# Performance work log

Hardware: AMD Instinct MI355X
Metric: run time of the kernel (lower is better)

Reference implementation:

```python
import jax, jax.numpy as jnp
import numpy as np

B, S, D, H = 1, 2048, 1024, 16
HD = D // H
THRESHOLD_PCT = 0.95
SPARSITY = 0.9
TOPK = max(1, int(S * (1.0 - SPARSITY)))  # 204


def setup_inputs() -> dict:
    key = jax.random.key(0)
    ks = jax.random.split(key, 6)
    inp = {
        'x': jax.random.normal(ks[0], (B, S, D), dtype=jnp.float32),
        'Wq': jax.random.normal(ks[1], (D, D), dtype=jnp.float32) * 0.02,
        'bq': jnp.zeros((D,), jnp.float32),
        'Wk': jax.random.normal(ks[2], (D, D), dtype=jnp.float32) * 0.02,
        'bk': jnp.zeros((D,), jnp.float32),
        'Wv': jax.random.normal(ks[3], (D, D), dtype=jnp.float32) * 0.02,
        'bv': jnp.zeros((D,), jnp.float32),
        'Wo': jax.random.normal(ks[4], (D, D), dtype=jnp.float32) * 0.02,
        'bo': jnp.zeros((D,), jnp.float32),
    }
    return inp


def _heads(t):  # [B,S,D] -> [B,H,S,HD]
    return t.reshape(B, S, H, HD).transpose(0, 2, 1, 3)


def reference(x, Wq, bq, Wk, bk, Wv, bv, Wo, bo):
    q = _heads(x @ Wq + bq)
    k = _heads(x @ Wk + bk)
    v = _heads(x @ Wv + bv)
    scores = jnp.einsum('bhqd,bhkd->bhqk', q, k) / jnp.sqrt(jnp.float32(HD))

    # --- dynamic threshold mask (per batch,head quantile over all S*S scores) ---
    flat = scores.reshape(B, H, S * S)
    thr = jnp.quantile(flat, THRESHOLD_PCT, axis=-1)[..., None, None]  # [B,H,1,1]
    thresh_mask = scores >= thr
    # fallback: if kept fraction exceeds (1 - sparsity_ratio), use per-row top-k
    cond = jnp.mean(thresh_mask.astype(scores.dtype)) > (1.0 - SPARSITY)
    kth = jax.lax.top_k(scores, TOPK)[0][..., -1:]  # k-th largest per row
    topk_mask = scores >= kth
    mask = jnp.where(cond, topk_mask, thresh_mask)

    masked = jnp.where(mask, scores, -jnp.inf)
    attn = jax.nn.softmax(masked, axis=-1)
    out = jnp.einsum('bhqk,bhkd->bhqd', attn, v)
    out = out.transpose(0, 2, 1, 3).reshape(B, S, D)
    return out @ Wo + bo
```

## Files before the change

### kernel.cpp

```cpp
#include <hip/hip_runtime.h>
#include <math.h>

#define SS 2048
#define DD 1024
#define HH 16
#define CAPC 49152u
#define LCAP 2048

#define K_A 3984587u
#define K_B 3984588u
#define QFRAC 0.85f
#define WSCALE 2048.0f
#define WSCALE_INV (1.0f/2048.0f)
#define ESHIFT 4.0f
#define PLANE 2097152

typedef _Float16 f16x8 __attribute__((ext_vector_type(8)));
typedef _Float16 f16x4 __attribute__((ext_vector_type(4)));
typedef float    f32x4 __attribute__((ext_vector_type(4)));

__device__ __forceinline__ unsigned sortkey(float f) {
  unsigned b = __float_as_uint(f);
  return (b & 0x80000000u) ? ~b : (b | 0x80000000u);
}
__device__ __forceinline__ float inv_sortkey(unsigned u) {
  unsigned b = (u & 0x80000000u) ? (u ^ 0x80000000u) : ~u;
  return __uint_as_float(b);
}

__global__ __launch_bounds__(256) void split_x(const float* __restrict__ x,
                                               _Float16* __restrict__ xh,
                                               _Float16* __restrict__ xl)
{
  const int i = blockIdx.x * 256 + threadIdx.x;
  float4 v = ((const float4*)x)[i];
  float vv[4] = {v.x, v.y, v.z, v.w};
  f16x4 h, l;
#pragma unroll
  for (int j = 0; j < 4; ++j) {
    _Float16 hh = (_Float16)vv[j];
    h[j] = hh;
    l[j] = (_Float16)(vv[j] - (float)hh);
  }
  ((f16x4*)xh)[i] = h;
  ((f16x4*)xl)[i] = l;
}

__global__ __launch_bounds__(256) void split_wT(const float* __restrict__ Wq,
                                                const float* __restrict__ Wk,
                                                const float* __restrict__ Wv,
                                                const float* __restrict__ Wo,
                                                _Float16* __restrict__ wplanes)
{
  const int z = blockIdx.z;
  const float* W = (z == 0) ? Wq : (z == 1) ? Wk : (z == 2) ? Wv : Wo;
  _Float16* WhT = wplanes + (size_t)(2*z)     * (1024*1024);
  _Float16* WlT = wplanes + (size_t)(2*z + 1) * (1024*1024);
  __shared__ float tile[64][65];
  const int t  = threadIdx.x;
  const int r  = t >> 2;
  const int c0 = (t & 3) * 16;
  const int k0 = blockIdx.y * 64;
  const int n0 = blockIdx.x * 64;
#pragma unroll
  for (int j = 0; j < 4; ++j) {
    float4 v = *(const float4*)&W[(size_t)(k0 + r) * 1024 + n0 + c0 + j*4];
    tile[r][c0+j*4+0] = v.x; tile[r][c0+j*4+1] = v.y;
    tile[r][c0+j*4+2] = v.z; tile[r][c0+j*4+3] = v.w;
  }
  __syncthreads();
  f16x8 h0, h1, l0, l1;
#pragma unroll
  for (int j = 0; j < 8; ++j) {
    float v = tile[c0 + j][r] * WSCALE;
    _Float16 h = (_Float16)v;
    h0[j] = h; l0[j] = (_Float16)(v - (float)h);
  }
#pragma unroll
  for (int j = 0; j < 8; ++j) {
    float v = tile[c0 + 8 + j][r] * WSCALE;
    _Float16 h = (_Float16)v;
    h1[j] = h; l1[j] = (_Float16)(v - (float)h);
  }
  const size_t o = (size_t)(n0 + r) * 1024 + k0 + c0;
  *(f16x8*)&WhT[o]     = h0;
  *(f16x8*)&WhT[o + 8] = h1;
  *(f16x8*)&WlT[o]     = l0;
  *(f16x8*)&WlT[o + 8] = l1;
}

__device__ __forceinline__ void gemm_mfma_part(const _Float16* __restrict__ Ah,
                                               const _Float16* __restrict__ Al,
                                               const _Float16* __restrict__ BhT,
                                               const _Float16* __restrict__ BlT,
                                               float* __restrict__ pout,
                                               int bm, int bn, int kh)
{
  const int wave = threadIdx.x >> 6, lane = threadIdx.x & 63;
  const int wr = wave >> 1, wc = wave & 1;
  const int m0 = bm * 128 + wr * 64;
  const int n0 = bn * 128 + wc * 64;
  const int lr = lane & 15;
  const int ko = lane >> 4;

  f32x4 acc[4][4];
#pragma unroll
  for (int i = 0; i < 4; ++i)
#pragma unroll
    for (int j = 0; j < 4; ++j) acc[i][j] = (f32x4){0.f, 0.f, 0.f, 0.f};

  for (int kk = kh*16; kk < kh*16 + 16; ++kk) {
    const int kof = kk*32 + ko*8;
    f16x8 aH[4], aL[4], bH[4], bL[4];
#pragma unroll
    for (int i = 0; i < 4; ++i) {
      const size_t aoff = (size_t)(m0 + i*16 + lr) * 1024 + kof;
      aH[i] = *(const f16x8*)(Ah + aoff);
      aL[i] = *(const f16x8*)(Al + aoff);
      const size_t boff = (size_t)(n0 + i*16 + lr) * 1024 + kof;
      bH[i] = *(const f16x8*)(BhT + boff);
      bL[i] = *(const f16x8*)(BlT + boff);
    }
#pragma unroll
    for (int i = 0; i < 4; ++i)
#pragma unroll
      for (int j = 0; j < 4; ++j) {
        acc[i][j] = __builtin_amdgcn_mfma_f32_16x16x32_f16(aL[i], bL[j], acc[i][j], 0, 0, 0);
        acc[i][j] = __builtin_amdgcn_mfma_f32_16x16x32_f16(aH[i], bL[j], acc[i][j], 0, 0, 0);
        acc[i][j] = __builtin_amdgcn_mfma_f32_16x16x32_f16(aL[i], bH[j], acc[i][j], 0, 0, 0);
        acc[i][j] = __builtin_amdgcn_mfma_f32_16x16x32_f16(aH[i], bH[j], acc[i][j], 0, 0, 0);
      }
  }

#pragma unroll
  for (int i = 0; i < 4; ++i)
#pragma unroll
    for (int j = 0; j < 4; ++j)
#pragma unroll
      for (int r = 0; r < 4; ++r) {
        const int row = m0 + i*16 + ko*4 + r;
        const int col = n0 + j*16 + lr;
        pout[(size_t)row * 1024 + col] = acc[i][j][r];
      }
}

__global__ __launch_bounds__(256) void gemm_qkv_part(const _Float16* __restrict__ xh,
                                                     const _Float16* __restrict__ xl,
                                                     const _Float16* __restrict__ wplanes,
                                                     float* __restrict__ pbuf)
{
  const int z = blockIdx.z;
  const int g = z >> 1, kh = z & 1;
  const _Float16* BhT = wplanes + (size_t)(2*g)     * (1024*1024);
  const _Float16* BlT = wplanes + (size_t)(2*g + 1) * (1024*1024);
  gemm_mfma_part(xh, xl, BhT, BlT, pbuf + (size_t)z * PLANE,
                 blockIdx.y, blockIdx.x, kh);
}

__global__ __launch_bounds__(256) void gemm_o_part(const _Float16* __restrict__ ctxh,
                                                   const _Float16* __restrict__ ctxl,
                                                   const _Float16* __restrict__ wplanes,
                                                   float* __restrict__ pO)
{
  const int kh = blockIdx.z;
  gemm_mfma_part(ctxh, ctxl,
                 wplanes + (size_t)6 * (1024*1024),
                 wplanes + (size_t)7 * (1024*1024),
                 pO + (size_t)kh * PLANE, blockIdx.y, blockIdx.x, kh);
}

__global__ __launch_bounds__(256) void combine_qk(const float* __restrict__ pbuf,
                                                  const float* __restrict__ bq,
                                                  const float* __restrict__ bk,
                                                  _Float16* __restrict__ Qh,
                                                  _Float16* __restrict__ Ql,
                                                  _Float16* __restrict__ Kh,
                                                  _Float16* __restrict__ Kl)
{
  const int which = blockIdx.y;
  const float* p0 = pbuf + (size_t)(which*2)     * PLANE;
  const float* p1 = pbuf + (size_t)(which*2 + 1) * PLANE;
  const float* bias = which ? bk : bq;
  _Float16* Oh = which ? Kh : Qh;
  _Float16* Ol = which ? Kl : Ql;
  const int i = blockIdx.x * 256 + threadIdx.x;
  const int coloff = (i & 255) * 4;
  float4 a = ((const float4*)p0)[i];
  float4 b = ((const float4*)p1)[i];
  float av[4] = {a.x, a.y, a.z, a.w};
  float bv[4] = {b.x, b.y, b.z, b.w};
  f16x4 h, l;
#pragma unroll
  for (int j = 0; j < 4; ++j) {
    const float val = (av[j] + bv[j]) * WSCALE_INV + bias[coloff + j];
    _Float16 hh = (_Float16)val;
    h[j] = hh;
    l[j] = (_Float16)(val - (float)hh);
  }
  ((f16x4*)Oh)[i] = h;
  ((f16x4*)Ol)[i] = l;
}

__global__ __launch_bounds__(256) void combine_vT(const float* __restrict__ pbuf,
                                                  const float* __restrict__ bv,
                                                  _Float16* __restrict__ VtH,
                                                  _Float16* __restrict__ VtL)
{
  const float* p0 = pbuf + (size_t)4 * PLANE;
  const float* p1 = pbuf + (size_t)5 * PLANE;
  __shared__ float tile[64][65];
  const int t  = threadIdx.x;
  const int d0 = blockIdx.x * 64;
  const int m0 = blockIdx.y * 64;
  {
    const int r  = t >> 2;
    const int c0 = (t & 3) * 16;
#pragma unroll
    for (int j = 0; j < 4; ++j) {
      const size_t o = (size_t)(m0 + r) * 1024 + d0 + c0 + j*4;
      float4 a = *(const float4*)(p0 + o);
      float4 b = *(const float4*)(p1 + o);
      tile[r][c0+j*4+0] = (a.x + b.x) * WSCALE_INV + bv[d0 + c0 + j*4 + 0];
      tile[r][c0+j*4+1] = (a.y + b.y) * WSCALE_INV + bv[d0 + c0 + j*4 + 1];
      tile[r][c0+j*4+2] = (a.z + b.z) * WSCALE_INV + bv[d0 + c0 + j*4 + 2];
      tile[r][c0+j*4+3] = (a.w + b.w) * WSCALE_INV + bv[d0 + c0 + j*4 + 3];
    }
  }
  __syncthreads();
  {
    const int d  = t >> 2;
    const int rg = (t & 3) * 16;
#pragma unroll
    for (int j = 0; j < 4; ++j) {
      f16x4 hv, lv;
#pragma unroll
      for (int r = 0; r < 4; ++r) {
        const float val = tile[rg + j*4 + r][d];
        _Float16 h = (_Float16)val;
        hv[r] = h; lv[r] = (_Float16)(val - (float)h);
      }
      const size_t o = (size_t)(d0 + d) * 2048 + m0 + rg + j*4;
      *(f16x4*)&VtH[o] = hv;
      *(f16x4*)&VtL[o] = lv;
    }
  }
}

__global__ __launch_bounds__(256) void combine_o(const float* __restrict__ pO,
                                                 const float* __restrict__ bo,
                                                 float* __restrict__ out)
{
  const float* p0 = pO;
  const float* p1 = pO + (size_t)1 * PLANE;
  const int i = blockIdx.x * 256 + threadIdx.x;
  const int coloff = (i & 255) * 4;
  float4 a = ((const float4*)p0)[i];
  float4 b = ((const float4*)p1)[i];
  float4 o;
  o.x = (a.x + b.x) * WSCALE_INV + bo[coloff + 0];
  o.y = (a.y + b.y) * WSCALE_INV + bo[coloff + 1];
  o.z = (a.z + b.z) * WSCALE_INV + bo[coloff + 2];
  o.w = (a.w + b.w) * WSCALE_INV + bo[coloff + 3];
  ((float4*)out)[i] = o;
}

__global__ __launch_bounds__(256) void combine_ctx(const float* __restrict__ pctx,
                                                   const float* __restrict__ prs,
                                                   _Float16* __restrict__ ctxh,
                                                   _Float16* __restrict__ ctxl)
{
  const float* p0 = pctx;
  const float* p1 = pctx + (size_t)1 * PLANE;
  const int i = blockIdx.x * 256 + threadIdx.x;
  const int row = i >> 8;
  const int cd  = (i & 255) * 4;
  const int h   = cd >> 6;
  const float rs = prs[h*2048 + row] + prs[32768 + h*2048 + row];
  float4 a = ((const float4*)p0)[i];
  float4 b = ((const float4*)p1)[i];
  float av[4] = {a.x, a.y, a.z, a.w};
  float bv[4] = {b.x, b.y, b.z, b.w};
  f16x4 hh, ll;
#pragma unroll
  for (int j = 0; j < 4; ++j) {
    const float val = (av[j] + bv[j]) / rs;
    _Float16 hv = (_Float16)val;
    hh[j] = hv;
    ll[j] = (_Float16)(val - (float)hv);
  }
  ((f16x4*)ctxh)[i] = hh;
  ((f16x4*)ctxl)[i] = ll;
}

__global__ __launch_bounds__(512) void scores_hist(const _Float16* __restrict__ Qh,
                                                   const _Float16* __restrict__ Ql,
                                                   const _Float16* __restrict__ Kh,
                                                   const _Float16* __restrict__ Kl,
                                                   unsigned* __restrict__ ghist)
{
  const int bn = blockIdx.x, bm = blockIdx.y, h = blockIdx.z;
  const int wave = threadIdx.x >> 6, lane = threadIdx.x & 63;
  const int wr = wave >> 1, wc = wave & 1;
  const int m0 = bm * 256 + wr * 64;
  const int n0 = bn * 128 + wc * 64;
  const int lr = lane & 15;
  const int ko = lane >> 4;

  __shared__ unsigned lh[16384];
  for (int i = threadIdx.x; i < 16384; i += 512) lh[i] = 0;
  __syncthreads();

  f32x4 acc[4][4];
#pragma unroll
  for (int i = 0; i < 4; ++i)
#pragma unroll
    for (int j = 0; j < 4; ++j) acc[i][j] = (f32x4){0.f, 0.f, 0.f, 0.f};

#pragma unroll
  for (int kk = 0; kk < 2; ++kk) {
    f16x8 aH[4], aL[4], bH[4], bL[4];
#pragma unroll
    for (int i = 0; i < 4; ++i) {
      const size_t aoff = (size_t)(m0 + i*16 + lr) * 1024 + h*64 + kk*32 + ko*8;
      aH[i] = *(const f16x8*)(Qh + aoff);
      aL[i] = *(const f16x8*)(Ql + aoff);
      const size_t boff = (size_t)(n0 + i*16 + lr) * 1024 + h*64 + kk*32 + ko*8;
      bH[i] = *(const f16x8*)(Kh + boff);
      bL[i] = *(const f16x8*)(Kl + boff);
    }
#pragma unroll
    for (int i = 0; i < 4; ++i)
#pragma unroll
      for (int j = 0; j < 4; ++j) {
        acc[i][j] = __builtin_amdgcn_mfma_f32_16x16x32_f16(aL[i], bL[j], acc[i][j], 0, 0, 0);
        acc[i][j] = __builtin_amdgcn_mfma_f32_16x16x32_f16(aH[i], bL[j], acc[i][j], 0, 0, 0);
        acc[i][j] = __builtin_amdgcn_mfma_f32_16x16x32_f16(aL[i], bH[j], acc[i][j], 0, 0, 0);
        acc[i][j] = __builtin_amdgcn_mfma_f32_16x16x32_f16(aH[i], bH[j], acc[i][j], 0, 0, 0);
      }
  }

#pragma unroll
  for (int i = 0; i < 4; ++i)
#pragma unroll
    for (int j = 0; j < 4; ++j)
#pragma unroll
      for (int r = 0; r < 4; ++r) {
        const float val = acc[i][j][r] * 0.125f;
        atomicAdd(&lh[sortkey(val) >> 18], 1u);
      }
  __syncthreads();
  unsigned* __restrict__ gh = ghist + (size_t)h * 16384;
  for (int i = threadIdx.x; i < 16384; i += 512) {
    const unsigned c = lh[i];
    if (c) atomicAdd(&gh[i], c);
  }
}

__global__ __launch_bounds__(256) void init14(unsigned* __restrict__ ghist,
                                              unsigned* __restrict__ ccnt)
{
  int i = blockIdx.x * 256 + threadIdx.x;
  for (; i < HH * 16384; i += gridDim.x * 256) ghist[i] = 0;
  if (blockIdx.x == 0 && threadIdx.x < HH) ccnt[threadIdx.x] = 0;
}

__global__ __launch_bounds__(256) void scan14(const unsigned* __restrict__ ghist,
                                              unsigned* __restrict__ state)
{
  const int hh = blockIdx.x;
  const int t = threadIdx.x;
  __shared__ unsigned part[256];
  __shared__ unsigned out[4];
  const unsigned* __restrict__ hb = ghist + (size_t)hh * 16384;
  unsigned s = 0;
  for (int j = 0; j < 64; ++j) s += hb[t*64 + j];
  part[t] = s;
  __syncthreads();
  if (t == 0) {
    unsigned run = 0;
    for (int i = 0; i < 256; ++i) { unsigned tmp = part[i]; part[i] = run; run += tmp; }
  }
  __syncthreads();
  const unsigned cum0 = part[t];
  if (K_A >= cum0 && K_A < cum0 + s) {
    unsigned c2 = cum0;
    for (int j = 0; j < 64; ++j) {
      const unsigned c = hb[t*64 + j];
      if (K_A < c2 + c) {
        const unsigned binA = t*64 + j;
        const unsigned residA = K_A - c2;
        unsigned binB, residB;
        if (residA + 1 < c) { binB = binA; residB = residA + 1; }
        else {
          unsigned bb = binA + 1;
          while (bb < 16384 && hb[bb] == 0) ++bb;
          if (bb >= 16384) bb = 16383;
          binB = bb; residB = 0;
        }
        out[0] = binA; out[1] = residA; out[2] = binB; out[3] = residB;
        break;
      }
      c2 += c;
    }
  }
  __syncthreads();
  if (t < 4) state[hh*4 + t] = out[t];
}

__global__ __launch_bounds__(512) void compact_recompute(const _Float16* __restrict__ Qh,
                                                         const _Float16* __restrict__ Ql,
                                                         const _Float16* __restrict__ Kh,
                                                         const _Float16* __restrict__ Kl,
                                                         const unsigned* __restrict__ state,
                                                         unsigned* __restrict__ cand,
                                                         unsigned* __restrict__ ccnt)
{
  const int bn = blockIdx.x, bm = blockIdx.y, h = blockIdx.z;
  const int wave = threadIdx.x >> 6, lane = threadIdx.x & 63;
  const int wr = wave >> 1, wc = wave & 1;
  const int m0 = bm * 256 + wr * 64;
  const int n0 = bn * 128 + wc * 64;
  const int lr = lane & 15;
  const int ko = lane >> 4;

  __shared__ unsigned lbuf[LCAP];
  __shared__ unsigned lcnt, gbase;
  if (threadIdx.x == 0) lcnt = 0;
  __syncthreads();
  const unsigned binA = state[h*4+0];
  const unsigned binB = state[h*4+2];
  unsigned* __restrict__ mycand = cand + (size_t)h * CAPC;

  f32x4 acc[4][4];
#pragma unroll
  for (int i = 0; i < 4; ++i)
#pragma unroll
    for (int j = 0; j < 4; ++j) acc[i][j] = (f32x4){0.f, 0.f, 0.f, 0.f};

#pragma unroll
  for (int kk = 0; kk < 2; ++kk) {
    f16x8 aH[4], aL[4], bH[4], bL[4];
#pragma unroll
    for (int i = 0; i < 4; ++i) {
      const size_t aoff = (size_t)(m0 + i*16 + lr) * 1024 + h*64 + kk*32 + ko*8;
      aH[i] = *(const f16x8*)(Qh + aoff);
      aL[i] = *(const f16x8*)(Ql + aoff);
      const size_t boff = (size_t)(n0 + i*16 + lr) * 1024 + h*64 + kk*32 + ko*8;
      bH[i] = *(const f16x8*)(Kh + boff);
      bL[i] = *(const f16x8*)(Kl + boff);
    }
#pragma unroll
    for (int i = 0; i < 4; ++i)
#pragma unroll
      for (int j = 0; j < 4; ++j) {
        acc[i][j] = __builtin_amdgcn_mfma_f32_16x16x32_f16(aL[i], bL[j], acc[i][j], 0, 0, 0);
        acc[i][j] = __builtin_amdgcn_mfma_f32_16x16x32_f16(aH[i], bL[j], acc[i][j], 0, 0, 0);
        acc[i][j] = __builtin_amdgcn_mfma_f32_16x16x32_f16(aL[i], bH[j], acc[i][j], 0, 0, 0);
        acc[i][j] = __builtin_amdgcn_mfma_f32_16x16x32_f16(aH[i], bH[j], acc[i][j], 0, 0, 0);
      }
  }

#pragma unroll
  for (int i = 0; i < 4; ++i)
#pragma unroll
    for (int j = 0; j < 4; ++j)
#pragma unroll
      for (int r = 0; r < 4; ++r) {
        const float val = acc[i][j][r] * 0.125f;
        const unsigned u = sortkey(val);
        const unsigned bin = u >> 18;
        if (bin == binA || bin == binB) {
          unsigned id = atomicAdd(&lcnt, 1u);
          if (id < LCAP) lbuf[id] = u;
          else { unsigned g = atomicAdd(&ccnt[h], 1u); if (g < CAPC) mycand[g] = u; }
        }
      }
  __syncthreads();
  const unsigned n = (lcnt < LCAP) ? lcnt : LCAP;
  if (threadIdx.x == 0) gbase = n ? atomicAdd(&ccnt[h], n) : 0u;
  __syncthreads();
  const unsigned gb = gbase;
  for (unsigned i = threadIdx.x; i < n; i += 512)
    if (gb + i < CAPC) mycand[gb + i] = lbuf[i];
}

__global__ __launch_bounds__(256) void final_select_list(const unsigned* __restrict__ cand,
                                                         const unsigned* __restrict__ ccnt,
                                                         const unsigned* __restrict__ state,
                                                         float* __restrict__ thr)
{
  const int hh = blockIdx.x;
  const int t = threadIdx.x;
  __shared__ unsigned hist[256];
  __shared__ unsigned digitS, kresS;
  __shared__ float valS[2];
  unsigned n = ccnt[hh]; if (n > CAPC) n = CAPC;
  const unsigned* __restrict__ list = cand + (size_t)hh * CAPC;
  for (int tgt = 0; tgt < 2; ++tgt) {
    unsigned pfx = state[hh*4 + tgt*2];
    unsigned k   = state[hh*4 + tgt*2 + 1];
    for (int r = 0; r < 3; ++r) {
      const int s = (r == 0) ? 10 : (r == 1) ? 2 : 0;
      const int w = (r == 2) ? 2 : 8;
      const unsigned nb = 1u << w;
      hist[t] = 0;
      __syncthreads();
      for (unsigned i = t; i < n; i += 256) {
        const unsigned u = list[i];
        if ((u >> (s + w)) == pfx) atomicAdd(&hist[(u >> s) & (nb - 1)], 1u);
      }
      __syncthreads();
      if (t == 0) {
        unsigned cum = 0, b = 0;
        for (; b < nb; ++b) { const unsigned c = hist[b]; if (cum + c > k) break; cum += c; }
        if (b == nb) b = nb - 1;
        digitS = b; kresS = k - cum;
      }
      __syncthreads();
      pfx = (pfx << w) | digitS;
      k = kresS;
    }
    if (t == 0) valS[tgt] = inv_sortkey(pfx);
    __syncthreads();
  }
  if (t == 0) thr[hh] = valS[0] + QFRAC * (valS[1] - valS[0]);
}

__global__ __launch_bounds__(256) void flash_pv_sk(const _Float16* __restrict__ Qh,
                                                   const _Float16* __restrict__ Ql,
                                                   const _Float16* __restrict__ Kh,
                                                   const _Float16* __restrict__ Kl,
                                                   const _Float16* __restrict__ VtH,
                                                   const _Float16* __restrict__ VtL,
                                                   const float* __restrict__ thrArr,
                                                   float* __restrict__ pctx,
                                                   float* __restrict__ prs)
{
  const int bm = blockIdx.x;
  const int h  = blockIdx.y;
  const int half = blockIdx.z;
  const int wave = threadIdx.x >> 6, lane = threadIdx.x & 63;
  const int lr = lane & 15;
  const int ko = lane >> 4;
  const int m0 = bm * 64;
  const float thr = thrArr[h];

  __shared__ _Float16 Plds[64][136];
  __shared__ float rsLDS[64][4];

  f16x8 qH[4][2], qL[4][2];
#pragma unroll
  for (int i = 0; i < 4; ++i)
#pragma unroll
    for (int kk = 0; kk < 2; ++kk) {
      const size_t aoff = (size_t)(m0 + i*16 + lr) * 1024 + h*64 + kk*32 + ko*8;
      qH[i][kk] = *(const f16x8*)(Qh + aoff);
      qL[i][kk] = *(const f16x8*)(Ql + aoff);
    }

  f32x4 oacc[4];
#pragma unroll
  for (int i = 0; i < 4; ++i) oacc[i] = (f32x4){0.f, 0.f, 0.f, 0.f};
  float rs[4][4];
#pragma unroll
  for (int i = 0; i < 4; ++i)
#pragma unroll
    for (int r = 0; r < 4; ++r) rs[i][r] = 0.f;

  const int d0 = wave * 16;

  for (int kt = half*8; kt < half*8 + 8; ++kt) {
    const int n0 = kt*128 + wave*32;
    f32x4 sacc[4][2];
#pragma unroll
    for (int i = 0; i < 4; ++i)
#pragma unroll
      for (int j = 0; j < 2; ++j) sacc[i][j] = (f32x4){0.f, 0.f, 0.f, 0.f};

#pragma unroll
    for (int kk = 0; kk < 2; ++kk) {
      f16x8 bH[2], bL[2];
#pragma unroll
      for (int j = 0; j < 2; ++j) {
        const size_t boff = (size_t)(n0 + j*16 + lr) * 1024 + h*64 + kk*32 + ko*8;
        bH[j] = *(const f16x8*)(Kh + boff);
        bL[j] = *(const f16x8*)(Kl + boff);
      }
#pragma unroll
      for (int i = 0; i < 4; ++i)
#pragma unroll
        for (int j = 0; j < 2; ++j) {
          sacc[i][j] = __builtin_amdgcn_mfma_f32_16x16x32_f16(qL[i][kk], bL[j], sacc[i][j], 0, 0, 0);
          sacc[i][j] = __builtin_amdgcn_mfma_f32_16x16x32_f16(qH[i][kk], bL[j], sacc[i][j], 0, 0, 0);
          sacc[i][j] = __builtin_amdgcn_mfma_f32_16x16x32_f16(qL[i][kk], bH[j], sacc[i][j], 0, 0, 0);
          sacc[i][j] = __builtin_amdgcn_mfma_f32_16x16x32_f16(qH[i][kk], bH[j], sacc[i][j], 0, 0, 0);
        }
    }

#pragma unroll
    for (int i = 0; i < 4; ++i)
#pragma unroll
      for (int j = 0; j < 2; ++j)
#pragma unroll
        for (int r = 0; r < 4; ++r) {
          const float val = sacc[i][j][r] * 0.125f;
          const float p = (val >= thr) ? __expf(val - thr - ESHIFT) : 0.f;
          rs[i][r] += p;
          Plds[i*16 + ko*4 + r][wave*32 + j*16 + lr] = (_Float16)p;
        }
    __syncthreads();

#pragma unroll
    for (int kk2 = 0; kk2 < 4; ++kk2) {
      f16x8 pa[4];
#pragma unroll
      for (int i = 0; i < 4; ++i)
        pa[i] = *(const f16x8*)&Plds[i*16 + lr][kk2*32 + ko*8];
      const size_t vo = (size_t)(h*64 + d0 + lr) * 2048 + kt*128 + kk2*32 + ko*8;
      const f16x8 vH = *(const f16x8*)(VtH + vo);
      const f16x8 vL = *(const f16x8*)(VtL + vo);
#pragma unroll
      for (int i = 0; i < 4; ++i) {
        oacc[i] = __builtin_amdgcn_mfma_f32_16x16x32_f16(pa[i], vL, oacc[i], 0, 0, 0);
        oacc[i] = __builtin_amdgcn_mfma_f32_16x16x32_f16(pa[i], vH, oacc[i], 0, 0, 0);
      }
    }
    __syncthreads();
  }

#pragma unroll
  for (int i = 0; i < 4; ++i)
#pragma unroll
    for (int r = 0; r < 4; ++r) {
      float v = rs[i][r];
      v += __shfl_xor(v, 1); v += __shfl_xor(v, 2);
      v += __shfl_xor(v, 4); v += __shfl_xor(v, 8);
      rs[i][r] = v;
    }
  if (lr == 0) {
#pragma unroll
    for (int i = 0; i < 4; ++i)
#pragma unroll
      for (int r = 0; r < 4; ++r)
        rsLDS[i*16 + ko*4 + r][wave] = rs[i][r];
  }
  __syncthreads();

  if (wave == 0 && lr == 0) {
#pragma unroll
    for (int i = 0; i < 4; ++i)
#pragma unroll
      for (int r = 0; r < 4; ++r) {
        const int lrow = i*16 + ko*4 + r;
        prs[half*32768 + h*2048 + m0 + lrow] =
            rsLDS[lrow][0] + rsLDS[lrow][1] + rsLDS[lrow][2] + rsLDS[lrow][3];
      }
  }

  float* __restrict__ pc = pctx + (size_t)half * PLANE;
#pragma unroll
  for (int i = 0; i < 4; ++i)
#pragma unroll
    for (int r = 0; r < 4; ++r) {
      const int lrow = i*16 + ko*4 + r;
      pc[(size_t)(m0 + lrow) * 1024 + h*64 + d0 + lr] = oacc[i][r];
    }
}

extern "C" void kernel_launch(void* const* d_in, const int* in_sizes, int n_in,
                              void* d_out, int out_size, void* d_ws, size_t ws_size,
                              hipStream_t stream)
{
  const float* x  = (const float*)d_in[0];
  const float* Wq = (const float*)d_in[1];
  const float* bq = (const float*)d_in[2];
  const float* Wk = (const float*)d_in[3];
  const float* bk = (const float*)d_in[4];
  const float* Wv = (const float*)d_in[5];
  const float* bv = (const float*)d_in[6];
  const float* Wo = (const float*)d_in[7];
  const float* bo = (const float*)d_in[8];
  float* out = (float*)d_out;
  char*  ws  = (char*)d_ws;

  const size_t MB = 1u << 20;
  _Float16* xh      = (_Float16*)(ws + 0*MB);
  _Float16* xl      = (_Float16*)(ws + 4*MB);
  _Float16* wplanes = (_Float16*)(ws + 8*MB);
  _Float16* Qh      = (_Float16*)(ws + 24*MB);
  _Float16* Ql      = (_Float16*)(ws + 28*MB);
  _Float16* Kh      = (_Float16*)(ws + 32*MB);
  _Float16* Kl      = (_Float16*)(ws + 36*MB);
  _Float16* VtH     = (_Float16*)(ws + 40*MB);
  _Float16* VtL     = (_Float16*)(ws + 44*MB);
  _Float16* ctxh    = (_Float16*)(ws + 48*MB);
  _Float16* ctxl    = (_Float16*)(ws + 52*MB);
  const size_t base = 56*MB;
  unsigned* state = (unsigned*)(ws + base);
  float*    thr   = (float*)(ws + base + 4096);
  unsigned* ccnt  = (unsigned*)(ws + base + 8192);
  unsigned* ghist = (unsigned*)(ws + base + 16384);
  unsigned* cand  = (unsigned*)(ws + base + 16384 + 1048576);
  float*    prs   = (float*)(ws + 61*MB);
  float*    pbuf  = (float*)(ws + 64*MB);
  float*    pctx  = pbuf;
  float*    pO    = pbuf + (size_t)2 * PLANE;

  split_x<<<2048, 256, 0, stream>>>(x, xh, xl);
  split_wT<<<dim3(16, 16, 4), 256, 0, stream>>>(Wq, Wk, Wv, Wo, wplanes);
  gemm_qkv_part<<<dim3(8, 16, 6), 256, 0, stream>>>(xh, xl, wplanes, pbuf);
  combine_qk<<<dim3(2048, 2), 256, 0, stream>>>(pbuf, bq, bk, Qh, Ql, Kh, Kl);
  combine_vT<<<dim3(16, 32), 256, 0, stream>>>(pbuf, bv, VtH, VtL);

  init14<<<256, 256, 0, stream>>>(ghist, ccnt);
  scores_hist<<<dim3(16, 8, HH), 512, 0, stream>>>(Qh, Ql, Kh, Kl, ghist);
  scan14<<<HH, 256, 0, stream>>>(ghist, state);
  compact_recompute<<<dim3(16, 8, HH), 512, 0, stream>>>(Qh, Ql, Kh, Kl, state, cand, ccnt);
  final_select_list<<<HH, 256, 0, stream>>>(cand, ccnt, state, thr);
  flash_pv_sk<<<dim3(32, HH, 2), 256, 0, stream>>>(Qh, Ql, Kh, Kl, VtH, VtL, thr, pctx, prs);
  combine_ctx<<<2048, 256, 0, stream>>>(pctx, prs, ctxh, ctxl);

  gemm_o_part<<<dim3(8, 16, 2), 256, 0, stream>>>(ctxh, ctxl, wplanes, pO);
  combine_o<<<2048, 256, 0, stream>>>(pO, bo, out);
}
```

Before: 578.7 us.

## Predict quantile bin range via sampled histogram, compact candidates in one pass

Adds a sampling pass that computes scores for a strided subset of query rows to estimate the quantile bin per head, then fuses the full histogram with candidate compaction for bins in a window around that estimate. This removes the second full QK^T recompute in the common case. A check kernel verifies that the true quantile bins fall inside the predicted window and otherwise triggers the original fallback compaction. The cost is a larger candidate buffer, more atomics in the histogram kernel, and three extra small launches.

```diff
diff --git a/kernel.cpp b/kernel.cpp
--- a/kernel.cpp
+++ b/kernel.cpp
@@ -4,8 +4,9 @@
 #define SS 2048
 #define DD 1024
 #define HH 16
-#define CAPC 49152u
+#define CAPC 327680u
 #define LCAP 2048
+#define RBIN 4
 
 #define K_A 3984587u
 #define K_B 3984588u
@@ -14,6 +15,7 @@
 #define WSCALE_INV (1.0f/2048.0f)
 #define ESHIFT 4.0f
 #define PLANE 2097152
+#define NSAMP_RANK 124518u
 
 typedef _Float16 f16x8 __attribute__((ext_vector_type(8)));
 typedef _Float16 f16x4 __attribute__((ext_vector_type(4)));
@@ -292,11 +294,125 @@
   ((f16x4*)ctxl)[i] = ll;
 }
 
-__global__ __launch_bounds__(512) void scores_hist(const _Float16* __restrict__ Qh,
+__global__ __launch_bounds__(256) void init_sel(unsigned* __restrict__ ghist,
+                                                unsigned* __restrict__ shist,
+                                                unsigned* __restrict__ ccnt,
+                                                unsigned* __restrict__ flag)
+{
+  int i = blockIdx.x * 256 + threadIdx.x;
+  for (; i < HH * 16384; i += gridDim.x * 256) { ghist[i] = 0; shist[i] = 0; }
+  if (blockIdx.x == 0 && threadIdx.x < HH) { ccnt[threadIdx.x] = 0; flag[threadIdx.x] = 0; }
+}
+
+__global__ __launch_bounds__(256) void sample_hist(const _Float16* __restrict__ Qh,
                                                    const _Float16* __restrict__ Ql,
                                                    const _Float16* __restrict__ Kh,
                                                    const _Float16* __restrict__ Kl,
-                                                   unsigned* __restrict__ ghist)
+                                                   unsigned* __restrict__ shist)
+{
+  const int kb = blockIdx.x, h = blockIdx.y;
+  const int wave = threadIdx.x >> 6, lane = threadIdx.x & 63;
+  const int lr = lane & 15, ko = lane >> 4;
+  const int n0 = kb*128 + wave*32;
+
+  __shared__ unsigned lh[16384];
+  for (int i = threadIdx.x; i < 16384; i += 256) lh[i] = 0;
+  __syncthreads();
+
+  f32x4 acc[4][2];
+#pragma unroll
+  for (int i = 0; i < 4; ++i)
+#pragma unroll
+    for (int j = 0; j < 2; ++j) acc[i][j] = (f32x4){0.f, 0.f, 0.f, 0.f};
+
+#pragma unroll
+  for (int kk = 0; kk < 2; ++kk) {
+    f16x8 aH[4], aL[4], bH[2], bL[2];
+#pragma unroll
+    for (int i = 0; i < 4; ++i) {
+      const size_t aoff = (size_t)((i*16 + lr) * 32) * 1024 + h*64 + kk*32 + ko*8;
+      aH[i] = *(const f16x8*)(Qh + aoff);
+      aL[i] = *(const f16x8*)(Ql + aoff);
+    }
+#pragma unroll
+    for (int j = 0; j < 2; ++j) {
+      const size_t boff = (size_t)(n0 + j*16 + lr) * 1024 + h*64 + kk*32 + ko*8;
+      bH[j] = *(const f16x8*)(Kh + boff);
+      bL[j] = *(const f16x8*)(Kl + boff);
+    }
+#pragma unroll
+    for (int i = 0; i < 4; ++i)
+#pragma unroll
+      for (int j = 0; j < 2; ++j) {
+        acc[i][j] = __builtin_amdgcn_mfma_f32_16x16x32_f16(aL[i], bL[j], acc[i][j], 0, 0, 0);
+        acc[i][j] = __builtin_amdgcn_mfma_f32_16x16x32_f16(aH[i], bL[j], acc[i][j], 0, 0, 0);
+        acc[i][j] = __builtin_amdgcn_mfma_f32_16x16x32_f16(aL[i], bH[j], acc[i][j], 0, 0, 0);
+        acc[i][j] = __builtin_amdgcn_mfma_f32_16x16x32_f16(aH[i], bH[j], acc[i][j], 0, 0, 0);
+      }
+  }
+
+#pragma unroll
+  for (int i = 0; i < 4; ++i)
+#pragma unroll
+    for (int j = 0; j < 2; ++j)
+#pragma unroll
+      for (int r = 0; r < 4; ++r) {
+        const float val = acc[i][j][r] * 0.125f;
+        atomicAdd(&lh[sortkey(val) >> 18], 1u);
+      }
+  __syncthreads();
+  unsigned* __restrict__ gh = shist + (size_t)h * 16384;
+  for (int i = threadIdx.x; i < 16384; i += 256) {
+    const unsigned c = lh[i];
+    if (c) atomicAdd(&gh[i], c);
+  }
+}
+
+__global__ __launch_bounds__(256) void sample_scan(const unsigned* __restrict__ shist,
+                                                   unsigned* __restrict__ rangeLo,
+                                                   unsigned* __restrict__ rangeHi)
+{
+  const int hh = blockIdx.x;
+  const int t = threadIdx.x;
+  __shared__ unsigned part[256];
+  __shared__ unsigned outb;
+  if (t == 0) outb = 8192u;
+  const unsigned* __restrict__ hb = shist + (size_t)hh * 16384;
+  unsigned s = 0;
+  for (int j = 0; j < 64; ++j) s += hb[t*64 + j];
+  part[t] = s;
+  __syncthreads();
+  if (t == 0) {
+    unsigned run = 0;
+    for (int i = 0; i < 256; ++i) { unsigned tmp = part[i]; part[i] = run; run += tmp; }
+  }
+  __syncthreads();
+  const unsigned cum0 = part[t];
+  if (NSAMP_RANK >= cum0 && NSAMP_RANK < cum0 + s) {
+    unsigned c2 = cum0;
+    for (int j = 0; j < 64; ++j) {
+      const unsigned c = hb[t*64 + j];
+      if (NSAMP_RANK < c2 + c) { outb = t*64 + j; break; }
+      c2 += c;
+    }
+  }
+  __syncthreads();
+  if (t == 0) {
+    const int b = (int)outb;
+    rangeLo[hh] = (unsigned)((b - RBIN < 0) ? 0 : b - RBIN);
+    rangeHi[hh] = (unsigned)((b + RBIN > 16383) ? 16383 : b + RBIN);
+  }
+}
+
+__global__ __launch_bounds__(512) void hist_compact_range(const _Float16* __restrict__ Qh,
+                                                          const _Float16* __restrict__ Ql,
+                                                          const _Float16* __restrict__ Kh,
+                                                          const _Float16* __restrict__ Kl,
+                                                          unsigned* __restrict__ ghist,
+                                                          const unsigned* __restrict__ rangeLo,
+                                                          const unsigned* __restrict__ rangeHi,
+                                                          unsigned* __restrict__ cand,
+                                                          unsigned* __restrict__ ccnt)
 {
   const int bn = blockIdx.x, bm = blockIdx.y, h = blockIdx.z;
   const int wave = threadIdx.x >> 6, lane = threadIdx.x & 63;
@@ -305,9 +421,14 @@
   const int n0 = bn * 128 + wc * 64;
   const int lr = lane & 15;
   const int ko = lane >> 4;
+  const unsigned lo = rangeLo[h], hi = rangeHi[h];
+  unsigned* __restrict__ mycand = cand + (size_t)h * CAPC;
 
   __shared__ unsigned lh[16384];
+  __shared__ unsigned lbuf[LCAP];
+  __shared__ unsigned lcnt, gbase;
   for (int i = threadIdx.x; i < 16384; i += 512) lh[i] = 0;
+  if (threadIdx.x == 0) lcnt = 0;
   __syncthreads();
 
   f32x4 acc[4][4];
@@ -346,7 +467,14 @@
 #pragma unroll
       for (int r = 0; r < 4; ++r) {
         const float val = acc[i][j][r] * 0.125f;
-        atomicAdd(&lh[sortkey(val) >> 18], 1u);
+        const unsigned u = sortkey(val);
+        const unsigned bin = u >> 18;
+        atomicAdd(&lh[bin], 1u);
+        if (bin >= lo && bin <= hi) {
+          unsigned id = atomicAdd(&lcnt, 1u);
+          if (id < LCAP) lbuf[id] = u;
+          else { unsigned g = atomicAdd(&ccnt[h], 1u); if (g < CAPC) mycand[g] = u; }
+        }
       }
   __syncthreads();
   unsigned* __restrict__ gh = ghist + (size_t)h * 16384;
@@ -354,14 +482,12 @@
     const unsigned c = lh[i];
     if (c) atomicAdd(&gh[i], c);
   }
-}
-
-__global__ __launch_bounds__(256) void init14(unsigned* __restrict__ ghist,
-                                              unsigned* __restrict__ ccnt)
-{
-  int i = blockIdx.x * 256 + threadIdx.x;
-  for (; i < HH * 16384; i += gridDim.x * 256) ghist[i] = 0;
-  if (blockIdx.x == 0 && threadIdx.x < HH) ccnt[threadIdx.x] = 0;
+  const unsigned n = (lcnt < LCAP) ? lcnt : LCAP;
+  if (threadIdx.x == 0) gbase = n ? atomicAdd(&ccnt[h], n) : 0u;
+  __syncthreads();
+  const unsigned gb = gbase;
+  for (unsigned i = threadIdx.x; i < n; i += 512)
+    if (gb + i < CAPC) mycand[gb + i] = lbuf[i];
 }
 
 __global__ __launch_bounds__(256) void scan14(const unsigned* __restrict__ ghist,
@@ -407,15 +533,35 @@
   if (t < 4) state[hh*4 + t] = out[t];
 }
 
-__global__ __launch_bounds__(512) void compact_recompute(const _Float16* __restrict__ Qh,
-                                                         const _Float16* __restrict__ Ql,
-                                                         const _Float16* __restrict__ Kh,
-                                                         const _Float16* __restrict__ Kl,
-                                                         const unsigned* __restrict__ state,
-                                                         unsigned* __restrict__ cand,
-                                                         unsigned* __restrict__ ccnt)
+__global__ __launch_bounds__(64) void check_range(const unsigned* __restrict__ state,
+                                                  const unsigned* __restrict__ rangeLo,
+                                                  const unsigned* __restrict__ rangeHi,
+                                                  unsigned* __restrict__ ccnt,
+                                                  unsigned* __restrict__ flag)
+{
+  const int t = threadIdx.x;
+  if (t < HH) {
+    const unsigned binA = state[t*4+0];
+    const unsigned binB = state[t*4+2];
+    const unsigned lo = rangeLo[t], hi = rangeHi[t];
+    const unsigned ok = (binA >= lo && binA <= hi && binB >= lo && binB <= hi &&
+                         ccnt[t] <= CAPC) ? 1u : 0u;
+    flag[t] = ok;
+    if (!ok) ccnt[t] = 0;
+  }
+}
+
+__global__ __launch_bounds__(512) void fallback_compact(const _Float16* __restrict__ Qh,
+                                                        const _Float16* __restrict__ Ql,
+                                                        const _Float16* __restrict__ Kh,
+                                                        const _Float16* __restrict__ Kl,
+                                                        const unsigned* __restrict__ state,
+                                                        const unsigned* __restrict__ flagArr,
+                                                        unsigned* __restrict__ cand,
+                                                        unsigned* __restrict__ ccnt)
 {
   const int bn = blockIdx.x, bm = blockIdx.y, h = blockIdx.z;
+  if (flagArr[h] != 0) return;
   const int wave = threadIdx.x >> 6, lane = threadIdx.x & 63;
   const int wr = wave >> 1, wc = wave & 1;
   const int m0 = bm * 256 + wr * 64;
@@ -696,15 +842,19 @@
   _Float16* ctxh    = (_Float16*)(ws + 48*MB);
   _Float16* ctxl    = (_Float16*)(ws + 52*MB);
   const size_t base = 56*MB;
-  unsigned* state = (unsigned*)(ws + base);
-  float*    thr   = (float*)(ws + base + 4096);
-  unsigned* ccnt  = (unsigned*)(ws + base + 8192);
-  unsigned* ghist = (unsigned*)(ws + base + 16384);
-  unsigned* cand  = (unsigned*)(ws + base + 16384 + 1048576);
-  float*    prs   = (float*)(ws + 61*MB);
-  float*    pbuf  = (float*)(ws + 64*MB);
-  float*    pctx  = pbuf;
-  float*    pO    = pbuf + (size_t)2 * PLANE;
+  unsigned* state   = (unsigned*)(ws + base);
+  float*    thr     = (float*)(ws + base + 4096);
+  unsigned* ccnt    = (unsigned*)(ws + base + 8192);
+  unsigned* flag    = (unsigned*)(ws + base + 12288);
+  unsigned* rangeLo = (unsigned*)(ws + base + 16384);
+  unsigned* rangeHi = (unsigned*)(ws + base + 20480);
+  unsigned* ghist   = (unsigned*)(ws + 57*MB);
+  unsigned* shist   = (unsigned*)(ws + 58*MB);
+  unsigned* cand    = (unsigned*)(ws + 59*MB);
+  float*    prs     = (float*)(ws + 80*MB);
+  float*    pbuf    = (float*)(ws + 81*MB);
+  float*    pctx    = pbuf;
+  float*    pO      = pbuf + (size_t)2 * PLANE;
 
   split_x<<<2048, 256, 0, stream>>>(x, xh, xl);
   split_wT<<<dim3(16, 16, 4), 256, 0, stream>>>(Wq, Wk, Wv, Wo, wplanes);
@@ -712,10 +862,14 @@
   combine_qk<<<dim3(2048, 2), 256, 0, stream>>>(pbuf, bq, bk, Qh, Ql, Kh, Kl);
   combine_vT<<<dim3(16, 32), 256, 0, stream>>>(pbuf, bv, VtH, VtL);
 
-  init14<<<256, 256, 0, stream>>>(ghist, ccnt);
-  scores_hist<<<dim3(16, 8, HH), 512, 0, stream>>>(Qh, Ql, Kh, Kl, ghist);
+  init_sel<<<256, 256, 0, stream>>>(ghist, shist, ccnt, flag);
+  sample_hist<<<dim3(16, HH), 256, 0, stream>>>(Qh, Ql, Kh, Kl, shist);
+  sample_scan<<<HH, 256, 0, stream>>>(shist, rangeLo, rangeHi);
+  hist_compact_range<<<dim3(16, 8, HH), 512, 0, stream>>>(Qh, Ql, Kh, Kl, ghist,
+                                                          rangeLo, rangeHi, cand, ccnt);
   scan14<<<HH, 256, 0, stream>>>(ghist, state);
-  compact_recompute<<<dim3(16, 8, HH), 512, 0, stream>>>(Qh, Ql, Kh, Kl, state, cand, ccnt);
+  check_range<<<1, 64, 0, stream>>>(state, rangeLo, rangeHi, ccnt, flag);
+  fallback_compact<<<dim3(16, 8, HH), 512, 0, stream>>>(Qh, Ql, Kh, Kl, state, flag, cand, ccnt);
   final_select_list<<<HH, 256, 0, stream>>>(cand, ccnt, state, thr);
   flash_pv_sk<<<dim3(32, HH, 2), 256, 0, stream>>>(Qh, Ql, Kh, Kl, VtH, VtL, thr, pctx, prs);
   combine_ctx<<<2048, 256, 0, stream>>>(pctx, prs, ctxh, ctxl);
```

Measured after the change: 1.078 ms. +86.3%, slower.
